# Kernel optimization log

Hardware: AMD Instinct MI355X
Metric: run time of the kernel (lower is better)

The kernel has to match this reference:

```python
import jax, jax.numpy as jnp
import numpy as np

THRESHOLD = 1.0
DECAY = 0.95
T, B, N_IN = 16, 512, 3072
S1, S2, S3 = 256, 256, 128
E = 8


def _lif_step(v, h):
    # LIF membrane update: decay, integrate, threshold-spike, soft reset.
    v = v * DECAY + h
    spk = (v >= THRESHOLD).astype(v.dtype)
    return spk, v - spk * THRESHOLD


def setup_inputs() -> dict:
    key = jax.random.key(0)
    k_seq, k1, k2, k3 = jax.random.split(key, 4)
    # Binary spike train input (rate-coded), shape (T, B, N_in)
    spike_seq = (jax.random.uniform(k_seq, (T, B, N_IN)) < 0.5).astype(jnp.float32)
    # Expert weights: nn.Linear weight layout is (out, in); init N(0, 0.05)
    W1 = 0.05 * jax.random.normal(k1, (E, S1, N_IN), dtype=jnp.float32)
    W2 = 0.05 * jax.random.normal(k2, (E, S2, S1), dtype=jnp.float32)
    W3 = 0.05 * jax.random.normal(k3, (E, S3, S2), dtype=jnp.float32)
    # Uniform gates 1/num_experts (requires_grad=False buffers in the original)
    g = jnp.full((E,), 1.0 / E, dtype=jnp.float32)
    return {"spike_seq": spike_seq, "W1": W1, "W2": W2, "W3": W3,
            "g1": g, "g2": g, "g3": g}


def reference(spike_seq, W1, W2, W3, g1, g2, g3):
    t, b = spike_seq.shape[0], spike_seq.shape[1]
    x = spike_seq.reshape(t, b, -1)
    e = W1.shape[0]
    dt = x.dtype
    v1 = jnp.zeros((e, b, W1.shape[1]), dt)
    v2 = jnp.zeros((e, b, W2.shape[1]), dt)
    v3 = jnp.zeros((e, b, W3.shape[1]), dt)

    def step(carry, xt):
        v1, v2, v3 = carry
        # stage 1: batched per-expert GEMM + LIF + gated combine
        h1 = jnp.einsum('bi,eoi->ebo', xt, W1)
        spk1, v1 = _lif_step(v1, h1)
        c1 = jnp.einsum('e,ebo->bo', g1, spk1)
        # stage 2
        h2 = jnp.einsum('bi,eoi->ebo', c1, W2)
        spk2, v2 = _lif_step(v2, h2)
        c2 = jnp.einsum('e,ebo->bo', g2, spk2)
        # stage 3
        h3 = jnp.einsum('bi,eoi->ebo', c2, W3)
        spk3, v3 = _lif_step(v3, h3)
        c3 = jnp.einsum('e,ebo->bo', g3, spk3)
        return (v1, v2, v3), (c1, c2, c3)

    _, (s1, s2, s3) = jax.lax.scan(step, (v1, v2, v3), x)
    # time-averaged combined outputs per stage
    return s1.mean(axis=0), s2.mean(axis=0), s3.mean(axis=0)
```

## Files before the change

### kernel.cpp

```cpp
#include <hip/hip_runtime.h>
#include <hip/hip_bf16.h>
#include <cmath>

#define T_STEPS 16
#define BATCH   512
#define N_IN    3072
#define S1      256
#define S2      256
#define S3      128
#define NEXP    8
#define M_ROWS  (T_STEPS * BATCH)
#define MT_ALL  (M_ROWS / 32)

typedef int v4i  __attribute__((ext_vector_type(4)));
typedef int v16i __attribute__((ext_vector_type(16)));
typedef unsigned long long u64;
typedef unsigned int uint32;

__device__ __forceinline__ v4i unpack16_bits(uint32 w16)
{
    v4i d;
    #pragma unroll
    for (int c = 0; c < 4; ++c) {
        uint32 x = (w16 >> (4 * c)) & 0xFu;
        x = x + (x << 7);
        x = x + (x << 14);
        d[c] = (int)(x & 0x01010101u);
    }
    return d;
}

template<int S, int K>
__device__ __forceinline__ void digitize_chunk(
    const float* __restrict__ W, char* __restrict__ Bf, int t)
{
    int lane16 = t & 63;
    int o  = (t >> 6) & (S - 1);
    int kb = t >> ((S == 256) ? 14 : 13);
    int r  = lane16 & 31;
    int qd = lane16 >> 5;
    int e    = r >> 2;
    int limb = r & 3;
    int k0 = kb * 32 + qd * 16;

    const float4* Wp = (const float4*)(W + ((size_t)e * S + o) * K + k0);
    char out[16];
    #pragma unroll
    for (int f4 = 0; f4 < 4; ++f4) {
        float4 w = Wp[f4];
        float ws[4] = {w.x, w.y, w.z, w.w};
        #pragma unroll
        for (int c = 0; c < 4; ++c) {
            long long q = llrint((double)ws[c] * 4294967296.0);
            int d = 0;
            #pragma unroll
            for (int l = 0; l < 4; ++l) {
                int dl = (int)((q + 128) & 255) - 128;
                q = (q - dl) >> 8;
                if (l == limb) d = dl;
            }
            out[f4 * 4 + c] = (char)d;
        }
    }
    *(v4i*)(Bf + (size_t)t * 16) = *(v4i*)out;
}

__global__ __launch_bounds__(256) void prep(
    const float* __restrict__ x,  const float* __restrict__ W1,
    const float* __restrict__ W2, const float* __restrict__ W3,
    u64* __restrict__ bitsT, char* __restrict__ B1f,
    char* __restrict__ B2f,  char* __restrict__ B3f)
{
    const int bid = blockIdx.x;
    const int tid = threadIdx.x;
    if (bid < 98304) {
        int gid = bid * 256 + tid;
        float v = x[gid];
        u64 m = __ballot(v >= 0.5f);
        if ((tid & 63) == 0) {
            int tb = gid / N_IN;
            int k  = gid - tb * N_IN;
            int t  = tb >> 9;
            int b  = tb & 511;
            bitsT[(size_t)(k >> 6) * M_ROWS + (b * 16 + t)] = m;
        }
    } else if (bid < 98304 + 6144) {
        digitize_chunk<S1, N_IN>(W1, B1f, (bid - 98304) * 256 + tid);
    } else if (bid < 98304 + 6144 + 512) {
        digitize_chunk<S2, S1>(W2, B2f, (bid - 98304 - 6144) * 256 + tid);
    } else {
        digitize_chunk<S3, S2>(W3, B3f, (bid - 98304 - 6656) * 256 + tid);
    }
}

template<int K, int S, int SHIFT, bool ABITS, bool WRITEC, int NBLK, int MINW>
__global__ __launch_bounds__(256, MINW) void fused_stage(
    const void* __restrict__ Ap, const char* __restrict__ Bf,
    const float* __restrict__ g, char* __restrict__ Cf,
    float* __restrict__ Mean)
{
    constexpr int KI = K / 64;
    constexpr int NT = S;
    constexpr int NS = NBLK / 8;
    static_assert(M_ROWS / 256 == 32, "mblk count must be 32");
    __shared__ double hs[256][16];

    const int tid  = threadIdx.x;
    const int lane = tid & 63;
    const int w    = tid >> 6;
    const int col  = lane & 31;
    const int qd   = lane >> 5;
    const int wm   = w * 64;

    const int id    = blockIdx.x;
    const int xcd   = id & 7;
    const int inner = id >> 3;
    const int nblk  = xcd * NS + (inner >> 5);
    const int mblk  = inner & 31;
    const int m0    = mblk * 256;

    const int nt0 = nblk * 2;
    const char* Bbase = Bf + ((size_t)nt0 * 64 + lane) * 16;

    v16i acc[2][2];
    #pragma unroll
    for (int i = 0; i < 2; ++i)
        #pragma unroll
        for (int j = 0; j < 2; ++j)
            #pragma unroll
            for (int r = 0; r < 16; ++r) acc[i][j][r] = 0;

    auto loadB = [&](int kb, int jj) -> v4i {
        return *(const v4i*)(Bbase + (size_t)kb * (NT * 1024) + jj * 1024);
    };

    if constexpr (ABITS) {
        static_assert(!ABITS || KI % 3 == 0, "bits path wants KI % 3 == 0");
        const u64* AT = (const u64*)Ap + (m0 + wm + col);
        const int sh16 = qd * 16;
        u64 a0b[3], a1b[3];
        v4i Bb[3][4];

        #pragma unroll
        for (int s = 0; s < 2; ++s) {
            a0b[s] = AT[(size_t)s * M_ROWS];
            a1b[s] = AT[(size_t)s * M_ROWS + 32];
            #pragma unroll
            for (int ks = 0; ks < 2; ++ks)
                #pragma unroll
                for (int jj = 0; jj < 2; ++jj)
                    Bb[s][ks * 2 + jj] = loadB(s * 2 + ks, jj);
        }

        auto body = [&](int it, int cur, int pf) {
            const int itp = it + 2;
            a0b[pf] = AT[(size_t)itp * M_ROWS];
            a1b[pf] = AT[(size_t)itp * M_ROWS + 32];
            #pragma unroll
            for (int ks = 0; ks < 2; ++ks)
                #pragma unroll
                for (int jj = 0; jj < 2; ++jj)
                    Bb[pf][ks * 2 + jj] = loadB(itp * 2 + ks, jj);
            __builtin_amdgcn_s_setprio(1);
            #pragma unroll
            for (int ks = 0; ks < 2; ++ks) {
                uint32 dw0 = ks ? (uint32)(a0b[cur] >> 32) : (uint32)a0b[cur];
                uint32 dw1 = ks ? (uint32)(a1b[cur] >> 32) : (uint32)a1b[cur];
                v4i af0 = unpack16_bits(dw0 >> sh16);
                v4i af1 = unpack16_bits(dw1 >> sh16);
                #pragma unroll
                for (int jj = 0; jj < 2; ++jj) {
                    acc[0][jj] = __builtin_amdgcn_mfma_i32_32x32x32_i8(af0, Bb[cur][ks*2+jj], acc[0][jj], 0,0,0);
                    acc[1][jj] = __builtin_amdgcn_mfma_i32_32x32x32_i8(af1, Bb[cur][ks*2+jj], acc[1][jj], 0,0,0);
                }
            }
            __builtin_amdgcn_s_setprio(0);
        };
        for (int it = 0; it < KI; it += 3) {
            body(it + 0, 0, 2);
            body(it + 1, 1, 0);
            body(it + 2, 2, 1);
        }
    } else {
        static_assert(ABITS || KI % 2 == 0, "frag path wants even KI");
        const int mt0 = (m0 + wm) >> 5;
        const char* Abase = (const char*)Ap + ((size_t)mt0 * 64 + lane) * 16;
        auto loadA = [&](int kb, int ii) -> v4i {
            return *(const v4i*)(Abase + (size_t)kb * (MT_ALL * 1024) + ii * 1024);
        };
        v4i Ab[2][4];
        v4i Bb[2][4];

        #pragma unroll
        for (int ks = 0; ks < 2; ++ks) {
            Ab[0][ks * 2 + 0] = loadA(ks, 0);
            Ab[0][ks * 2 + 1] = loadA(ks, 1);
            #pragma unroll
            for (int jj = 0; jj < 2; ++jj)
                Bb[0][ks * 2 + jj] = loadB(ks, jj);
        }

        auto body = [&](int it, int cur, int pf) {
            const int itp = it + 1;
            #pragma unroll
            for (int ks = 0; ks < 2; ++ks) {
                Ab[pf][ks * 2 + 0] = loadA(itp * 2 + ks, 0);
                Ab[pf][ks * 2 + 1] = loadA(itp * 2 + ks, 1);
                #pragma unroll
                for (int jj = 0; jj < 2; ++jj)
                    Bb[pf][ks * 2 + jj] = loadB(itp * 2 + ks, jj);
            }
            #pragma unroll
            for (int ks = 0; ks < 2; ++ks)
                #pragma unroll
                for (int jj = 0; jj < 2; ++jj) {
                    acc[0][jj] = __builtin_amdgcn_mfma_i32_32x32x32_i8(Ab[cur][ks*2+0], Bb[cur][ks*2+jj], acc[0][jj], 0,0,0);
                    acc[1][jj] = __builtin_amdgcn_mfma_i32_32x32x32_i8(Ab[cur][ks*2+1], Bb[cur][ks*2+jj], acc[1][jj], 0,0,0);
                }
        };
        for (int it = 0; it < KI; it += 2) {
            body(it + 0, 0, 1);
            body(it + 1, 1, 0);
        }
    }

    const double sbase = 1.0 / (double)(1ll << SHIFT);
    #pragma unroll
    for (int j = 0; j < 2; ++j) {
        const int oe = j * 8 + (col >> 2);
        #pragma unroll
        for (int i = 0; i < 2; ++i) {
            #pragma unroll
            for (int reg = 0; reg < 16; ++reg) {
                int a = acc[i][j][reg];
                int s01 = a + (__shfl_xor(a, 1) << 8);
                int s23 = __shfl_xor(s01, 2);
                double d = ((double)s01 + 65536.0 * (double)s23) * sbase;
                if ((col & 3) == 0) {
                    int m = wm + i * 32 + (reg & 3) + 8 * (reg >> 2) + 4 * qd;
                    hs[m][oe] = d;
                }
            }
        }
    }
    __syncthreads();

    const int b_loc  = tid >> 4;
    const int o_loc  = (tid >> 3) & 1;
    const int e      = tid & 7;
    const int oe     = o_loc * 8 + e;
    const float ge   = g[e];
    const int bg = mblk * 16 + b_loc;
    const int og = nblk * 2 + o_loc;

    const int kb_a   = og >> 5;
    const int qd_a   = (og >> 4) & 1;
    const int byte_a = og & 15;

    double v = 0.0;
    float gacc = 0.0f;
    #pragma unroll
    for (int t = 0; t < T_STEPS; ++t) {
        double h  = hs[b_loc * 16 + t][oe];
        double vv = v * 0.95 + h;
        int spk = (vv >= 1.0) ? 1 : 0;
        v = vv - (double)spk;
        float gs = ge * (float)spk;
        gs += __shfl_xor(gs, 1);
        gs += __shfl_xor(gs, 2);
        gs += __shfl_xor(gs, 4);
        gacc += gs;
        if (WRITEC) {
            int cnt = spk;
            cnt += __shfl_xor(cnt, 1);
            cnt += __shfl_xor(cnt, 2);
            cnt += __shfl_xor(cnt, 4);
            if (e == 0) {
                int mp = bg * 16 + t;
                int lane_a = (mp & 31) + 32 * qd_a;
                Cf[(((size_t)kb_a * MT_ALL + (mp >> 5)) * 64 + lane_a) * 16 + byte_a]
                    = (char)cnt;
            }
        }
    }
    if (e == 0) Mean[(size_t)bg * S + og] = gacc * 0.0625f;
}

extern "C" void kernel_launch(void* const* d_in, const int* in_sizes, int n_in,
                              void* d_out, int out_size, void* d_ws, size_t ws_size,
                              hipStream_t stream) {
    const float* x  = (const float*)d_in[0];
    const float* W1 = (const float*)d_in[1];
    const float* W2 = (const float*)d_in[2];
    const float* W3 = (const float*)d_in[3];
    const float* g1 = (const float*)d_in[4];
    const float* g2 = (const float*)d_in[5];
    const float* g3 = (const float*)d_in[6];
    float* out = (float*)d_out;

    char* ws = (char*)d_ws;
    u64*  AbitsT = (u64*)ws;
    char* B1f    = ws + 4194304ull;
    char* B2f    = ws + 31457280ull;
    char* B3f    = ws + 34603008ull;
    char* c1f    = ws + 36175872ull;
    char* c2f    = ws + 39321600ull;

    dim3 blk(256);

    prep<<<98304 + 6144 + 512 + 256, blk, 0, stream>>>(
        x, W1, W2, W3, AbitsT, B1f, B2f, B3f);

    fused_stage<N_IN, S1, 32, true,  true,  128, 3><<<32 * 128, blk, 0, stream>>>(
        AbitsT, B1f, g1, c1f, out);
    fused_stage<S1,   S2, 35, false, true,  128, 3><<<32 * 128, blk, 0, stream>>>(
        c1f, B2f, g2, c2f, out + BATCH * S1);
    fused_stage<S2,   S3, 35, false, false, 64, 3><<<32 * 64, blk, 0, stream>>>(
        c2f, B3f, g3, nullptr, out + BATCH * (S1 + S2));
}
```

Measured before the change: 514.1 us.

## Use 3-limb int8 digitization for W1 with dedicated stage-1 kernel

Stage 1 weights are now quantized at 2^24 scale into three signed int8 limbs instead of the previous four-limb scheme. This shrinks the B1 fragment buffer and the number of MFMAs per output. A new dedicated stage-1 kernel recombines limbs with shifted 64-bit LDS atomics, then runs the LIF scan per (batch, output, expert). It also changes the tile shape to 128 rows by 3 column tiles. The precision drop from 32-bit to 24-bit scaling risks spike-threshold mismatches, and the LDS atomics add contention.

```diff
diff --git a/kernel.cpp b/kernel.cpp
--- a/kernel.cpp
+++ b/kernel.cpp
@@ -84,25 +84,197 @@
             int b  = tb & 511;
             bitsT[(size_t)(k >> 6) * M_ROWS + (b * 16 + t)] = m;
         }
-    } else if (bid < 98304 + 6144) {
-        digitize_chunk<S1, N_IN>(W1, B1f, (bid - 98304) * 256 + tid);
-    } else if (bid < 98304 + 6144 + 512) {
-        digitize_chunk<S2, S1>(W2, B2f, (bid - 98304 - 6144) * 256 + tid);
+    } else if (bid < 98304 + 4608) {
+        int t    = (bid - 98304) * 256 + tid;
+        int l16  = t & 63;
+        int tt   = t >> 6;
+        int tile = tt % 192;
+        int kb   = tt / 192;
+        int gr   = tile * 32 + (l16 & 31);
+        int qd   = l16 >> 5;
+        int o    = gr / 24;
+        int rem  = gr - o * 24;
+        int e    = rem / 3;
+        int limb = rem - e * 3;
+        int k0   = kb * 32 + qd * 16;
+        const float4* Wp = (const float4*)(W1 + ((size_t)e * S1 + o) * N_IN + k0);
+        char out[16];
+        #pragma unroll
+        for (int f4 = 0; f4 < 4; ++f4) {
+            float4 w = Wp[f4];
+            float ws[4] = {w.x, w.y, w.z, w.w};
+            #pragma unroll
+            for (int c = 0; c < 4; ++c) {
+                long long q = llrint((double)ws[c] * 16777216.0);
+                int d0 = (int)((q + 128) & 255) - 128;
+                long long q1 = (q - d0) >> 8;
+                int d1 = (int)((q1 + 128) & 255) - 128;
+                int d2 = (int)((q1 - d1) >> 8);
+                int d  = (limb == 0) ? d0 : ((limb == 1) ? d1 : d2);
+                out[f4 * 4 + c] = (char)d;
+            }
+        }
+        *(v4i*)(B1f + (size_t)t * 16) = *(v4i*)out;
+    } else if (bid < 98304 + 4608 + 512) {
+        digitize_chunk<S2, S1>(W2, B2f, (bid - 98304 - 4608) * 256 + tid);
     } else {
-        digitize_chunk<S3, S2>(W3, B3f, (bid - 98304 - 6656) * 256 + tid);
-    }
-}
-
-template<int K, int S, int SHIFT, bool ABITS, bool WRITEC, int NBLK, int MINW>
+        digitize_chunk<S3, S2>(W3, B3f, (bid - 98304 - 4608 - 512) * 256 + tid);
+    }
+}
+
+__global__ __launch_bounds__(256, 3) void fused_stage1(
+    const u64* __restrict__ AT0, const char* __restrict__ Bf,
+    const float* __restrict__ g, char* __restrict__ Cf,
+    float* __restrict__ Mean)
+{
+    constexpr int KI    = N_IN / 64;
+    constexpr int NTILES = 192;
+    constexpr int BSTEP = 2 * NTILES * 1024;
+    constexpr int KSOFF = NTILES * 1024;
+    __shared__ long long hsI[128 * 32];
+
+    const int tid  = threadIdx.x;
+    const int lane = tid & 63;
+    const int w    = tid >> 6;
+    const int col  = lane & 31;
+    const int qd   = lane >> 5;
+    const int wm   = w * 32;
+
+    #pragma unroll
+    for (int i = 0; i < 16; ++i) hsI[tid + i * 256] = 0;
+    __syncthreads();
+
+    const int id    = blockIdx.x;
+    const int xcd   = id & 7;
+    const int inner = id >> 3;
+    const int nblk  = xcd * 8 + (inner >> 6);
+    const int mblk  = inner & 63;
+    const int m0    = mblk * 128;
+
+    const u64* AT = AT0 + (m0 + wm + col);
+    const int sh16 = qd * 16;
+    const char* Bu = Bf + (size_t)nblk * 3 * 1024 + lane * 16;
+
+    v16i acc[3];
+    #pragma unroll
+    for (int j = 0; j < 3; ++j)
+        #pragma unroll
+        for (int r = 0; r < 16; ++r) acc[j][r] = 0;
+
+    u64 ab[3];
+    v4i Bb[3][6];
+
+    #pragma unroll
+    for (int s = 0; s < 2; ++s) {
+        ab[s] = AT[(size_t)s * M_ROWS];
+        const char* bu = Bu + (size_t)s * BSTEP;
+        #pragma unroll
+        for (int ks = 0; ks < 2; ++ks)
+            #pragma unroll
+            for (int jj = 0; jj < 3; ++jj)
+                Bb[s][ks * 3 + jj] = *(const v4i*)(bu + ks * KSOFF + jj * 1024);
+    }
+
+    auto body = [&](int it, int cur, int pf) {
+        const int itp = it + 2;
+        ab[pf] = AT[(size_t)itp * M_ROWS];
+        const char* bu = Bu + (size_t)itp * BSTEP;
+        #pragma unroll
+        for (int ks = 0; ks < 2; ++ks)
+            #pragma unroll
+            for (int jj = 0; jj < 3; ++jj)
+                Bb[pf][ks * 3 + jj] = *(const v4i*)(bu + ks * KSOFF + jj * 1024);
+        __builtin_amdgcn_s_setprio(1);
+        #pragma unroll
+        for (int ks = 0; ks < 2; ++ks) {
+            uint32 dw = ks ? (uint32)(ab[cur] >> 32) : (uint32)ab[cur];
+            v4i af = unpack16_bits(dw >> sh16);
+            #pragma unroll
+            for (int jj = 0; jj < 3; ++jj)
+                acc[jj] = __builtin_amdgcn_mfma_i32_32x32x32_i8(
+                    af, Bb[cur][ks * 3 + jj], acc[jj], 0, 0, 0);
+        }
+        __builtin_amdgcn_s_setprio(0);
+    };
+
+    for (int it = 0; it < KI; it += 3) {
+        __builtin_amdgcn_s_barrier();
+        body(it + 0, 0, 2);
+        body(it + 1, 1, 0);
+        body(it + 2, 2, 1);
+    }
+
+    int ocol[3], lsh[3];
+    #pragma unroll
+    for (int jj = 0; jj < 3; ++jj) {
+        int grb   = jj * 32 + col;
+        int o_rel = grb / 24;
+        int rem   = grb - o_rel * 24;
+        int e_    = rem / 3;
+        int limb  = rem - e_ * 3;
+        ocol[jj]  = o_rel * 8 + e_;
+        lsh[jj]   = limb * 8;
+    }
+    #pragma unroll
+    for (int jj = 0; jj < 3; ++jj)
+        #pragma unroll
+        for (int reg = 0; reg < 16; ++reg) {
+            int m = wm + (reg & 3) + 8 * (reg >> 2) + 4 * qd;
+            atomicAdd((unsigned long long*)&hsI[m * 32 + ocol[jj]],
+                      (unsigned long long)((long long)acc[jj][reg] << lsh[jj]));
+        }
+    __syncthreads();
+
+    const int b_loc = tid >> 5;
+    const int oe    = tid & 31;
+    const int o_loc = oe >> 3;
+    const int e     = tid & 7;
+    const float ge  = g[e];
+    const int bg = mblk * 8 + b_loc;
+    const int og = nblk * 4 + o_loc;
+
+    const int kb_a   = og >> 5;
+    const int qd_a   = (og >> 4) & 1;
+    const int byte_a = og & 15;
+
+    const double sc = 1.0 / 16777216.0;
+    double v = 0.0;
+    float gacc = 0.0f;
+    #pragma unroll
+    for (int t = 0; t < T_STEPS; ++t) {
+        double h  = (double)hsI[(b_loc * 16 + t) * 32 + oe] * sc;
+        double vv = v * 0.95 + h;
+        int spk = (vv >= 1.0) ? 1 : 0;
+        v = vv - (double)spk;
+        float gs = ge * (float)spk;
+        gs += __shfl_xor(gs, 1);
+        gs += __shfl_xor(gs, 2);
+        gs += __shfl_xor(gs, 4);
+        gacc += gs;
+        int cnt = spk;
+        cnt += __shfl_xor(cnt, 1);
+        cnt += __shfl_xor(cnt, 2);
+        cnt += __shfl_xor(cnt, 4);
+        if (e == 0) {
+            int mp = bg * 16 + t;
+            int lane_a = (mp & 31) + 32 * qd_a;
+            Cf[(((size_t)kb_a * MT_ALL + (mp >> 5)) * 64 + lane_a) * 16 + byte_a]
+                = (char)cnt;
+        }
+    }
+    if (e == 0) Mean[(size_t)bg * S1 + og] = gacc * 0.0625f;
+}
+
+template<int K, int S, int SHIFT, bool WRITEC, int NBLK, int MINW>
 __global__ __launch_bounds__(256, MINW) void fused_stage(
-    const void* __restrict__ Ap, const char* __restrict__ Bf,
+    const char* __restrict__ Ap, const char* __restrict__ Bf,
     const float* __restrict__ g, char* __restrict__ Cf,
     float* __restrict__ Mean)
 {
     constexpr int KI = K / 64;
+    static_assert(KI % 2 == 0, "frag path wants even KI");
     constexpr int NT = S;
     constexpr int NS = NBLK / 8;
-    static_assert(M_ROWS / 256 == 32, "mblk count must be 32");
     __shared__ double hs[256][16];
 
     const int tid  = threadIdx.x;
@@ -133,95 +305,45 @@
     auto loadB = [&](int kb, int jj) -> v4i {
         return *(const v4i*)(Bbase + (size_t)kb * (NT * 1024) + jj * 1024);
     };
-
-    if constexpr (ABITS) {
-        static_assert(!ABITS || KI % 3 == 0, "bits path wants KI % 3 == 0");
-        const u64* AT = (const u64*)Ap + (m0 + wm + col);
-        const int sh16 = qd * 16;
-        u64 a0b[3], a1b[3];
-        v4i Bb[3][4];
-
-        #pragma unroll
-        for (int s = 0; s < 2; ++s) {
-            a0b[s] = AT[(size_t)s * M_ROWS];
-            a1b[s] = AT[(size_t)s * M_ROWS + 32];
-            #pragma unroll
-            for (int ks = 0; ks < 2; ++ks)
-                #pragma unroll
-                for (int jj = 0; jj < 2; ++jj)
-                    Bb[s][ks * 2 + jj] = loadB(s * 2 + ks, jj);
-        }
-
-        auto body = [&](int it, int cur, int pf) {
-            const int itp = it + 2;
-            a0b[pf] = AT[(size_t)itp * M_ROWS];
-            a1b[pf] = AT[(size_t)itp * M_ROWS + 32];
-            #pragma unroll
-            for (int ks = 0; ks < 2; ++ks)
-                #pragma unroll
-                for (int jj = 0; jj < 2; ++jj)
-                    Bb[pf][ks * 2 + jj] = loadB(itp * 2 + ks, jj);
-            __builtin_amdgcn_s_setprio(1);
-            #pragma unroll
-            for (int ks = 0; ks < 2; ++ks) {
-                uint32 dw0 = ks ? (uint32)(a0b[cur] >> 32) : (uint32)a0b[cur];
-                uint32 dw1 = ks ? (uint32)(a1b[cur] >> 32) : (uint32)a1b[cur];
-                v4i af0 = unpack16_bits(dw0 >> sh16);
-                v4i af1 = unpack16_bits(dw1 >> sh16);
-                #pragma unroll
-                for (int jj = 0; jj < 2; ++jj) {
-                    acc[0][jj] = __builtin_amdgcn_mfma_i32_32x32x32_i8(af0, Bb[cur][ks*2+jj], acc[0][jj], 0,0,0);
-                    acc[1][jj] = __builtin_amdgcn_mfma_i32_32x32x32_i8(af1, Bb[cur][ks*2+jj], acc[1][jj], 0,0,0);
-                }
+    const int mt0 = (m0 + wm) >> 5;
+    const char* Abase = Ap + ((size_t)mt0 * 64 + lane) * 16;
+    auto loadA = [&](int kb, int ii) -> v4i {
+        return *(const v4i*)(Abase + (size_t)kb * (MT_ALL * 1024) + ii * 1024);
+    };
+
+    v4i Ab[2][4];
+    v4i Bb[2][4];
+
+    #pragma unroll
+    for (int ks = 0; ks < 2; ++ks) {
+        Ab[0][ks * 2 + 0] = loadA(ks, 0);
+        Ab[0][ks * 2 + 1] = loadA(ks, 1);
+        #pragma unroll
+        for (int jj = 0; jj < 2; ++jj)
+            Bb[0][ks * 2 + jj] = loadB(ks, jj);
+    }
+
+    auto body = [&](int it, int cur, int pf) {
+        const int itp = it + 1;
+        #pragma unroll
+        for (int ks = 0; ks < 2; ++ks) {
+            Ab[pf][ks * 2 + 0] = loadA(itp * 2 + ks, 0);
+            Ab[pf][ks * 2 + 1] = loadA(itp * 2 + ks, 1);
+            #pragma unroll
+            for (int jj = 0; jj < 2; ++jj)
+                Bb[pf][ks * 2 + jj] = loadB(itp * 2 + ks, jj);
+        }
+        #pragma unroll
+        for (int ks = 0; ks < 2; ++ks)
+            #pragma unroll
+            for (int jj = 0; jj < 2; ++jj) {
+                acc[0][jj] = __builtin_amdgcn_mfma_i32_32x32x32_i8(Ab[cur][ks*2+0], Bb[cur][ks*2+jj], acc[0][jj], 0,0,0);
+                acc[1][jj] = __builtin_amdgcn_mfma_i32_32x32x32_i8(Ab[cur][ks*2+1], Bb[cur][ks*2+jj], acc[1][jj], 0,0,0);
             }
-            __builtin_amdgcn_s_setprio(0);
-        };
-        for (int it = 0; it < KI; it += 3) {
-            body(it + 0, 0, 2);
-            body(it + 1, 1, 0);
-            body(it + 2, 2, 1);
-        }
-    } else {
-        static_assert(ABITS || KI % 2 == 0, "frag path wants even KI");
-        const int mt0 = (m0 + wm) >> 5;
-        const char* Abase = (const char*)Ap + ((size_t)mt0 * 64 + lane) * 16;
-        auto loadA = [&](int kb, int ii) -> v4i {
-            return *(const v4i*)(Abase + (size_t)kb * (MT_ALL * 1024) + ii * 1024);
-        };
-        v4i Ab[2][4];
-        v4i Bb[2][4];
-
-        #pragma unroll
-        for (int ks = 0; ks < 2; ++ks) {
-            Ab[0][ks * 2 + 0] = loadA(ks, 0);
-            Ab[0][ks * 2 + 1] = loadA(ks, 1);
-            #pragma unroll
-            for (int jj = 0; jj < 2; ++jj)
-                Bb[0][ks * 2 + jj] = loadB(ks, jj);
-        }
-
-        auto body = [&](int it, int cur, int pf) {
-            const int itp = it + 1;
-            #pragma unroll
-            for (int ks = 0; ks < 2; ++ks) {
-                Ab[pf][ks * 2 + 0] = loadA(itp * 2 + ks, 0);
-                Ab[pf][ks * 2 + 1] = loadA(itp * 2 + ks, 1);
-                #pragma unroll
-                for (int jj = 0; jj < 2; ++jj)
-                    Bb[pf][ks * 2 + jj] = loadB(itp * 2 + ks, jj);
-            }
-            #pragma unroll
-            for (int ks = 0; ks < 2; ++ks)
-                #pragma unroll
-                for (int jj = 0; jj < 2; ++jj) {
-                    acc[0][jj] = __builtin_amdgcn_mfma_i32_32x32x32_i8(Ab[cur][ks*2+0], Bb[cur][ks*2+jj], acc[0][jj], 0,0,0);
-                    acc[1][jj] = __builtin_amdgcn_mfma_i32_32x32x32_i8(Ab[cur][ks*2+1], Bb[cur][ks*2+jj], acc[1][jj], 0,0,0);
-                }
-        };
-        for (int it = 0; it < KI; it += 2) {
-            body(it + 0, 0, 1);
-            body(it + 1, 1, 0);
-        }
+    };
+    for (int it = 0; it < KI; it += 2) {
+        body(it + 0, 0, 1);
+        body(it + 1, 1, 0);
     }
 
     const double sbase = 1.0 / (double)(1ll << SHIFT);
@@ -301,20 +423,20 @@
     char* ws = (char*)d_ws;
     u64*  AbitsT = (u64*)ws;
     char* B1f    = ws + 4194304ull;
-    char* B2f    = ws + 31457280ull;
-    char* B3f    = ws + 34603008ull;
-    char* c1f    = ws + 36175872ull;
-    char* c2f    = ws + 39321600ull;
+    char* B2f    = ws + 25165824ull;
+    char* B3f    = ws + 28311552ull;
+    char* c1f    = ws + 30408704ull;
+    char* c2f    = ws + 34603008ull;
 
     dim3 blk(256);
 
-    prep<<<98304 + 6144 + 512 + 256, blk, 0, stream>>>(
+    prep<<<98304 + 4608 + 512 + 256, blk, 0, stream>>>(
         x, W1, W2, W3, AbitsT, B1f, B2f, B3f);
 
-    fused_stage<N_IN, S1, 32, true,  true,  128, 3><<<32 * 128, blk, 0, stream>>>(
-        AbitsT, B1f, g1, c1f, out);
-    fused_stage<S1,   S2, 35, false, true,  128, 3><<<32 * 128, blk, 0, stream>>>(
+    fused_stage1<<<64 * 64, blk, 0, stream>>>(AbitsT, B1f, g1, c1f, out);
+
+    fused_stage<S1, S2, 35, true,  128, 3><<<32 * 128, blk, 0, stream>>>(
         c1f, B2f, g2, c2f, out + BATCH * S1);
-    fused_stage<S2,   S3, 35, false, false, 64, 3><<<32 * 64, blk, 0, stream>>>(
+    fused_stage<S2, S3, 35, false, 64, 3><<<32 * 64, blk, 0, stream>>>(
         c2f, B3f, g3, nullptr, out + BATCH * (S1 + S2));
 }
```

Result: faster. 489.4 us (-4.8%).
